# Kernel optimization log

Hardware: AMD Instinct MI355X
Metric: run time of the kernel (lower is better)

## Reference

```python
import jax, jax.numpy as jnp
import numpy as np

B, C, H, W = 4, 64, 96, 320
K = 9  # 3x3 kernel points
EPS = 1e-5


def conv3x3(x, w, b):
    # x: [B,Cin,H,W], w: [Cout,Cin,3,3], stride 1, pad 1
    out = jax.lax.conv_general_dilated(
        x, w, window_strides=(1, 1), padding=[(1, 1), (1, 1)],
        dimension_numbers=("NCHW", "OIHW", "NCHW"))
    return out + b[None, :, None, None]


def bn_eval(x, gamma, beta, mean, var):
    scale = gamma / jnp.sqrt(var + EPS)
    return x * scale[None, :, None, None] + (beta - mean * scale)[None, :, None, None]


def mdcn(x, offset, mask, w, b):
    # Modulated deformable conv v2, kernel 3, stride 1, pad 1, dilation 1.
    # offset: [B,2K,H,W] (channel 2k = dy, 2k+1 = dx, mmcv layout); mask: [B,K,H,W]
    Bb, Cc, Hh, Ww = x.shape
    off = offset.reshape(Bb, K, 2, Hh, Ww)
    dy, dx = off[:, :, 0], off[:, :, 1]               # [B,K,H,W]
    ks = jnp.arange(K)
    ky = (ks // 3 - 1).astype(x.dtype)[None, :, None, None]  # kernel row offset (pad=1)
    kx = (ks % 3 - 1).astype(x.dtype)[None, :, None, None]
    py = jnp.arange(Hh, dtype=x.dtype)[None, None, :, None] + ky + dy  # sample y
    px = jnp.arange(Ww, dtype=x.dtype)[None, None, None, :] + kx + dx  # sample x
    y0 = jnp.floor(py); x0 = jnp.floor(px)
    wy = py - y0; wx = px - x0
    y0i = y0.astype(jnp.int32); x0i = x0.astype(jnp.int32)
    x_flat = x.reshape(Bb, Cc, Hh * Ww)

    def gather(yi, xi):
        # bilinear corner with zero padding outside the image
        valid = ((yi >= 0) & (yi < Hh) & (xi >= 0) & (xi < Ww)).astype(x.dtype)
        idx = (jnp.clip(yi, 0, Hh - 1) * Ww + jnp.clip(xi, 0, Ww - 1)).reshape(Bb, 1, K * Hh * Ww)
        v = jnp.take_along_axis(x_flat, idx, axis=2).reshape(Bb, Cc, K, Hh, Ww)
        return v * valid[:, None]

    val = (((1 - wy) * (1 - wx))[:, None] * gather(y0i, x0i)
           + ((1 - wy) * wx)[:, None] * gather(y0i, x0i + 1)
           + (wy * (1 - wx))[:, None] * gather(y0i + 1, x0i)
           + (wy * wx)[:, None] * gather(y0i + 1, x0i + 1))  # [B,C,K,H,W]
    val = val * mask[:, None]
    out = jnp.einsum('bckhw,ock->bohw', val, w.reshape(w.shape[0], Cc, K))
    return out + b[None, :, None, None]


def setup_inputs() -> dict:
    key = jax.random.key(0)
    ks = jax.random.split(key, 16)
    s = 0.05
    return {
        "feat_rgb": jax.random.normal(ks[0], (B, C, H, W), jnp.float32),
        "feat_depth": jax.random.normal(ks[1], (B, C, H, W), jnp.float32),
        "w_off1": jax.random.normal(ks[2], (C, C, 3, 3), jnp.float32) * s,
        "b_off1": jax.random.normal(ks[3], (C,), jnp.float32) * s,
        "g1": 1.0 + jax.random.normal(ks[4], (C,), jnp.float32) * 0.1,
        "be1": jax.random.normal(ks[5], (C,), jnp.float32) * 0.1,
        "m1": jax.random.normal(ks[6], (C,), jnp.float32) * 0.1,
        "v1": jax.random.uniform(ks[7], (C,), jnp.float32, 0.5, 1.5),
        "w_off2": jax.random.normal(ks[8], (3 * K, C, 3, 3), jnp.float32) * s,
        "b_off2": jax.random.normal(ks[9], (3 * K,), jnp.float32) * s,
        "w_def": jax.random.normal(ks[10], (C, C, 3, 3), jnp.float32) * s,
        "b_def": jax.random.normal(ks[11], (C,), jnp.float32) * s,
        "w_f1": jax.random.normal(ks[12], (C, 2 * C, 3, 3), jnp.float32) * s,
        "b_f1": jax.random.normal(ks[13], (C,), jnp.float32) * s,
        "g2": 1.0 + jax.random.normal(ks[14], (C,), jnp.float32) * 0.1,
        "be2": jax.random.normal(ks[15], (C,), jnp.float32) * 0.1,
        "m2": jax.random.normal(jax.random.fold_in(key, 101), (C,), jnp.float32) * 0.1,
        "v2": jax.random.uniform(jax.random.fold_in(key, 102), (C,), jnp.float32, 0.5, 1.5),
        "w_out": jax.random.normal(jax.random.fold_in(key, 103), (1, C, 3, 3), jnp.float32) * s,
        "b_out": jax.random.normal(jax.random.fold_in(key, 104), (1,), jnp.float32) * s,
    }


def reference(feat_rgb, feat_depth, w_off1, b_off1, g1, be1, m1, v1,
              w_off2, b_off2, w_def, b_def, w_f1, b_f1, g2, be2, m2, v2,
              w_out, b_out):
    # offset head
    t = conv3x3(feat_rgb, w_off1, b_off1)
    t = bn_eval(t, g1, be1, m1, v1)
    head = conv3x3(t, w_off2, b_off2)            # [B,27,H,W]
    o1, o2, msk = jnp.split(head, 3, axis=1)
    offset = jnp.concatenate([o1, o2], axis=1)   # [B,18,H,W]
    msk = jax.nn.sigmoid(msk)                    # [B,9,H,W]
    # modulated deformable conv on depth features
    deform = mdcn(feat_depth, offset, msk, w_def, b_def)
    fd = feat_depth + deform
    fusion = jnp.concatenate([fd, feat_rgb], axis=1)  # [B,2C,H,W]
    h = jax.nn.relu(fusion)
    h = conv3x3(h, w_f1, b_f1)
    h = bn_eval(h, g2, be2, m2, v2)
    h = jax.nn.relu(h)  # Dropout(0.1) is identity at eval
    return conv3x3(h, w_out, b_out)  # [B,1,H,W]
```

## Files before the change

### kernel.cpp

```cpp
#include <hip/hip_runtime.h>
#include <math.h>

constexpr int Bc  = 4;
constexpr int Hc  = 96;
constexpr int Wc  = 320;
constexpr int HWc = Hc * Wc;
constexpr int NPIX = Bc * HWc;

typedef __attribute__((ext_vector_type(8))) short short8;
typedef __attribute__((ext_vector_type(4))) float f32x4;

constexpr size_t B_W1   = 0;
constexpr size_t B_W2   = 73728;
constexpr size_t B_WD   = 110592;
constexpr size_t B_WF   = 184320;
constexpr size_t B_AB   = 331776;
constexpr size_t B_RGBT = 332800;
constexpr size_t B_DEPT = 16061440;
constexpr size_t B_TT   = 31790080;
constexpr size_t B_HEAD = 47518720;

static __device__ __forceinline__ unsigned short f2bf(float f) {
    unsigned u = __builtin_bit_cast(unsigned, f);
    u = (u + 0x7fffu + ((u >> 16) & 1u)) >> 16;
    return (unsigned short)u;
}
static __device__ __forceinline__ float bf2f(unsigned short h) {
    unsigned u = ((unsigned)h) << 16;
    return __builtin_bit_cast(float, u);
}
static __device__ __forceinline__ int swz_blk(int bid, int chunk) {
    return (bid & 7) * chunk + (bid >> 3);
}

__global__ void prep_w(const float* __restrict__ w1, const float* __restrict__ b1,
                       const float* __restrict__ g1, const float* __restrict__ be1,
                       const float* __restrict__ m1, const float* __restrict__ v1,
                       const float* __restrict__ w2,
                       const float* __restrict__ wd,
                       const float* __restrict__ wf, const float* __restrict__ bf1,
                       const float* __restrict__ g2, const float* __restrict__ be2,
                       const float* __restrict__ m2, const float* __restrict__ v2,
                       char* __restrict__ ws) {
    int tid = blockIdx.x * blockDim.x + threadIdx.x;
    int stride = gridDim.x * blockDim.x;
    unsigned short* W1 = (unsigned short*)(ws + B_W1);
    unsigned short* W2 = (unsigned short*)(ws + B_W2);
    unsigned short* WD = (unsigned short*)(ws + B_WD);
    unsigned short* WF = (unsigned short*)(ws + B_WF);
    float* AB = (float*)(ws + B_AB);
    for (int i = tid; i < 36864; i += stride) {
        int ci = i & 63, co = (i >> 6) & 63, kk = i >> 12;
        W1[i] = f2bf(w1[(co * 64 + ci) * 9 + kk]);
    }
    for (int i = tid; i < 18432; i += stride) {
        int ci = i & 63, co = (i >> 6) & 31, kk = i >> 11;
        W2[i] = (co < 27) ? f2bf(w2[(co * 64 + ci) * 9 + kk]) : (unsigned short)0;
    }
    for (int i = tid; i < 36864; i += stride) {
        int c = i & 63, o = (i >> 6) & 63, kk = i >> 12;
        WD[i] = f2bf(wd[(o * 64 + c) * 9 + kk]);
    }
    for (int i = tid; i < 73728; i += stride) {
        int ci = i & 63, co = (i >> 6) & 63, r = i >> 12;
        int kk = r % 9, h = r / 9;
        WF[i] = f2bf(wf[(co * 128 + h * 64 + ci) * 9 + kk]);
    }
    if (tid < 64) {
        float s1 = g1[tid] / sqrtf(v1[tid] + 1e-5f);
        AB[tid]        = s1;
        AB[64 + tid]   = b1[tid] * s1 + be1[tid] - m1[tid] * s1;
        float s2 = g2[tid] / sqrtf(v2[tid] + 1e-5f);
        AB[128 + tid]  = s2;
        AB[192 + tid]  = bf1[tid] * s2 + be2[tid] - m2[tid] * s2;
    }
}

__global__ __launch_bounds__(256) void prep_x2(const float* __restrict__ rgb,
                                               const float* __restrict__ dep,
                                               unsigned short* __restrict__ rgbT,
                                               unsigned short* __restrict__ depT) {
    __shared__ unsigned short tr[64 * 66];
    int pg0 = blockIdx.x * 64;
    int b = pg0 / HWc, pix0 = pg0 % HWc;
    const float* srcs[2] = { rgb, dep };
    unsigned short* dsts[2] = { rgbT, depT };
#pragma unroll
    for (int which = 0; which < 2; ++which) {
        if (which) __syncthreads();
        const float* src = srcs[which];
#pragma unroll
        for (int it = 0; it < 16; ++it) {
            int idx = it * 256 + threadIdx.x;
            int p = idx & 63, ch = idx >> 6;
            float v = src[((size_t)b * 64 + ch) * HWc + pix0 + p];
            tr[p * 66 + ch] = f2bf(v);
        }
        __syncthreads();
        unsigned short* dst = dsts[which];
#pragma unroll
        for (int it = 0; it < 2; ++it) {
            int q = it * 256 + threadIdx.x;
            int p = q >> 3, g = q & 7;
            const char* basep = (const char*)tr + p * 132 + g * 16;
            uint4 u;
            u.x = *(const unsigned*)(basep + 0);
            u.y = *(const unsigned*)(basep + 4);
            u.z = *(const unsigned*)(basep + 8);
            u.w = *(const unsigned*)(basep + 12);
            *(uint4*)(dst + (size_t)(pg0 + p) * 64 + g * 8) = u;
        }
    }
}

static __device__ __forceinline__ void stage6(const unsigned short* __restrict__ src,
                                              int b, int y0, int x0,
                                              unsigned short* lds, bool do_relu) {
#pragma unroll
    for (int it = 0; it < 13; ++it) {
        int i = threadIdx.x + it * 256;
        if (i < 3168) {
            int g = i & 7;
            int xx = (i >> 3) % 66;
            int row = (i >> 3) / 66;
            int y = y0 - 1 + row, x = x0 - 1 + xx;
            short8 v = (short8)0;
            if ((unsigned)y < 96u && (unsigned)x < 320u) {
                v = *(const short8*)(src + ((size_t)(b * HWc + y * Wc + x)) * 64 + g * 8);
            }
            if (do_relu) {
#pragma unroll
                for (int j = 0; j < 8; ++j) {
                    short s = v[j];
                    v[j] = (s & (short)0x8000) ? (short)0 : s;
                }
            }
            int byte = ((row * 66 + xx) * 64 + g * 8) * 2;
            byte ^= ((xx & 7) << 4);
            *(short8*)((char*)lds + byte) = v;
        }
    }
}

static __device__ __forceinline__ short8 read_b6(const unsigned short* lds, int row, int xx, int cofs) {
    int byte = ((row * 66 + xx) * 64 + cofs) * 2;
    byte ^= ((xx & 7) << 4);
    return *(const short8*)((const char*)lds + byte);
}

__global__ __launch_bounds__(256) void conv1_m(const unsigned short* __restrict__ rgbT,
                                               const char* __restrict__ ws,
                                               unsigned short* __restrict__ tT) {
    __shared__ __align__(16) unsigned short xls[6 * 66 * 64];
    const unsigned short* W1 = (const unsigned short*)(ws + B_W1);
    const float* AB = (const float*)(ws + B_AB);
    int blk = swz_blk(blockIdx.x, 60);
    int xt = blk % 5, yt = (blk / 5) % 24, b = blk / 120;
    int x0 = xt * 64, y0 = yt * 4;
    stage6(rgbT, b, y0, x0, xls, false);
    __syncthreads();
    int lane = threadIdx.x & 63, w = threadIdx.x >> 6;
    int pl = lane & 15, q4 = lane >> 4;
    int p = w * 16 + pl;
    f32x4 acc[4][4];
#pragma unroll
    for (int r = 0; r < 4; ++r)
#pragma unroll
        for (int cp = 0; cp < 4; ++cp) acc[r][cp] = (f32x4)0.f;
#pragma unroll
    for (int kk = 0; kk < 9; ++kk) {
        int dy = kk / 3, dx = kk % 3;
        int xx = p + dx;
#pragma unroll
        for (int ch = 0; ch < 2; ++ch) {
            short8 bfr[4];
#pragma unroll
            for (int r = 0; r < 4; ++r) bfr[r] = read_b6(xls, dy + r, xx, ch * 32 + q4 * 8);
#pragma unroll
            for (int cp = 0; cp < 4; ++cp) {
                short8 afr = *(const short8*)(W1 + ((kk * 64 + cp * 16 + pl) * 64 + ch * 32 + q4 * 8));
#pragma unroll
                for (int r = 0; r < 4; ++r)
                    acc[r][cp] = __builtin_amdgcn_mfma_f32_16x16x32_bf16(afr, bfr[r], acc[r][cp], 0, 0, 0);
            }
        }
    }
#pragma unroll
    for (int r = 0; r < 4; ++r) {
        size_t pglob = (size_t)(b * HWc + (y0 + r) * Wc + x0 + p);
#pragma unroll
        for (int cp = 0; cp < 4; ++cp) {
            int co0 = cp * 16 + q4 * 4;
            f32x4 a1 = *(const f32x4*)(AB + co0);
            f32x4 b1 = *(const f32x4*)(AB + 64 + co0);
            unsigned short h4[4];
#pragma unroll
            for (int j = 0; j < 4; ++j) h4[j] = f2bf(fmaf(acc[r][cp][j], a1[j], b1[j]));
            uint2 u;
            u.x = (unsigned)h4[0] | ((unsigned)h4[1] << 16);
            u.y = (unsigned)h4[2] | ((unsigned)h4[3] << 16);
            *(uint2*)(tT + pglob * 64 + co0) = u;
        }
    }
}

__global__ __launch_bounds__(256) void conv2_m(const char* __restrict__ ws,
                                               const float* __restrict__ b2,
                                               float* __restrict__ headT,
                                               const unsigned short* __restrict__ tT) {
    __shared__ __align__(16) unsigned short xls[6 * 66 * 64];
    const unsigned short* W2 = (const unsigned short*)(ws + B_W2);
    int blk = swz_blk(blockIdx.x, 60);
    int xt = blk % 5, yt = (blk / 5) % 24, b = blk / 120;
    int x0 = xt * 64, y0 = yt * 4;
    stage6(tT, b, y0, x0, xls, false);
    __syncthreads();
    int lane = threadIdx.x & 63, w = threadIdx.x >> 6;
    int pl = lane & 15, q4 = lane >> 4;
    int p = w * 16 + pl;
    f32x4 acc[4][2];
#pragma unroll
    for (int r = 0; r < 4; ++r) { acc[r][0] = (f32x4)0.f; acc[r][1] = (f32x4)0.f; }
#pragma unroll
    for (int kk = 0; kk < 9; ++kk) {
        int dy = kk / 3, dx = kk % 3;
        int xx = p + dx;
#pragma unroll
        for (int ch = 0; ch < 2; ++ch) {
            short8 bfr[4];
#pragma unroll
            for (int r = 0; r < 4; ++r) bfr[r] = read_b6(xls, dy + r, xx, ch * 32 + q4 * 8);
#pragma unroll
            for (int cp = 0; cp < 2; ++cp) {
                short8 afr = *(const short8*)(W2 + ((kk * 32 + cp * 16 + pl) * 64 + ch * 32 + q4 * 8));
#pragma unroll
                for (int r = 0; r < 4; ++r)
                    acc[r][cp] = __builtin_amdgcn_mfma_f32_16x16x32_bf16(afr, bfr[r], acc[r][cp], 0, 0, 0);
            }
        }
    }
#pragma unroll
    for (int r = 0; r < 4; ++r) {
        size_t pglob = (size_t)(b * HWc + (y0 + r) * Wc + x0 + p);
#pragma unroll
        for (int cp = 0; cp < 2; ++cp) {
            int co0 = cp * 16 + q4 * 4;
            f32x4 rr;
#pragma unroll
            for (int j = 0; j < 4; ++j) {
                float bias = (co0 + j < 27) ? b2[co0 + j] : 0.f;
                rr[j] = acc[r][cp][j] + bias;
            }
            *(f32x4*)(headT + pglob * 32 + co0) = rr;
        }
    }
}

__global__ __launch_bounds__(256) void mdcn_l(const unsigned short* __restrict__ depthT,
                                              const float* __restrict__ headT,
                                              const char* __restrict__ ws,
                                              const float* __restrict__ bd,
                                              unsigned short* __restrict__ fdreluT) {
    __shared__ __align__(16) unsigned short vls[26048];
    const unsigned short* WD = (const unsigned short*)(ws + B_WD);
    int blk = swz_blk(blockIdx.x, 240);
    int xt = blk % 5, y = (blk / 5) % 96, b = blk / 480;
    int x0 = xt * 64;
    int lane = threadIdx.x & 63, w = threadIdx.x >> 6;
    int pl = lane & 15, q4 = lane >> 4;
    int p = w * 16 + pl;
    int px = x0 + p;
    size_t pglob = (size_t)(b * HWc + y * Wc + px);
    size_t dbase = (size_t)b * HWc * 64;
    const float* hd = headT + pglob * 32;
    float hv[28];
#pragma unroll
    for (int i = 0; i < 7; ++i) {
        f32x4 t = *(const f32x4*)(hd + i * 4);
        hv[i * 4 + 0] = t[0]; hv[i * 4 + 1] = t[1];
        hv[i * 4 + 2] = t[2]; hv[i * 4 + 3] = t[3];
    }
    f32x4 acc[4];
#pragma unroll
    for (int cp = 0; cp < 4; ++cp) acc[cp] = (f32x4)0.f;

    const int wy0 = y - 5;
    const int wx0 = x0 - 5;

#pragma unroll
    for (int pass = 0; pass < 2; ++pass) {
        if (pass) __syncthreads();
#pragma unroll
        for (int it = 0; it < 13; ++it) {
            int i = threadIdx.x + it * 256;
            if (i < 3256) {
                int sub = i & 3;
                int c = (i >> 2) % 74;
                int r = (i >> 2) / 74;
                int gy = wy0 + r, gx = wx0 + c;
                short8 v = (short8)0;
                if ((unsigned)gy < 96u && (unsigned)gx < 320u)
                    v = *(const short8*)(depthT + ((size_t)(b * HWc + gy * Wc + gx)) * 64 + pass * 32 + sub * 8);
                int byte = (((r * 74 + c) * 64) + sub * 16) ^ ((c & 6) << 3);
                *(short8*)((char*)vls + byte) = v;
            }
        }
        __syncthreads();
#pragma unroll
        for (int kk = 0; kk < 9; ++kk) {
            float dyv = hv[2 * kk], dxv = hv[2 * kk + 1], sm = hv[18 + kk];
            float m = 1.f / (1.f + __expf(-sm));
            float py  = (float)(y + kk / 3 - 1) + dyv;
            float pxf = (float)(px + kk % 3 - 1) + dxv;
            float y0f = floorf(py), x0f = floorf(pxf);
            float wy = py - y0f, wx = pxf - x0f;
            int iy0 = (int)y0f, ix0 = (int)x0f;
            bool vy0 = (unsigned)iy0 < 96u, vy1 = (unsigned)(iy0 + 1) < 96u;
            bool vx0 = (unsigned)ix0 < 320u, vx1 = (unsigned)(ix0 + 1) < 320u;
            int cy0 = min(max(iy0, 0), 95),  cy1 = min(max(iy0 + 1, 0), 95);
            int cx0 = min(max(ix0, 0), 319), cx1 = min(max(ix0 + 1, 0), 319);
            float w00 = (vy0 && vx0) ? (1.f - wy) * (1.f - wx) * m : 0.f;
            float w01 = (vy0 && vx1) ? (1.f - wy) * wx * m : 0.f;
            float w10 = (vy1 && vx0) ? wy * (1.f - wx) * m : 0.f;
            float w11 = (vy1 && vx1) ? wy * wx * m : 0.f;
            bool inw = ((unsigned)(iy0 - wy0) <= 9u) && ((unsigned)(ix0 - wx0) <= 72u);
            int lr0 = min(max(cy0 - wy0, 0), 10), lr1 = min(max(cy1 - wy0, 0), 10);
            int lc0 = min(max(cx0 - wx0, 0), 73), lc1 = min(max(cx1 - wx0, 0), 73);
            int qb = q4 * 16;
            short8 f00 = *(const short8*)((const char*)vls + ((((lr0 * 74 + lc0) * 64) + qb) ^ ((lc0 & 6) << 3)));
            short8 f01 = *(const short8*)((const char*)vls + ((((lr0 * 74 + lc1) * 64) + qb) ^ ((lc1 & 6) << 3)));
            short8 f10 = *(const short8*)((const char*)vls + ((((lr1 * 74 + lc0) * 64) + qb) ^ ((lc0 & 6) << 3)));
            short8 f11 = *(const short8*)((const char*)vls + ((((lr1 * 74 + lc1) * 64) + qb) ^ ((lc1 & 6) << 3)));
            if (!__all(inw)) {
                if (!inw) {
                    const unsigned short* bp = depthT + dbase + pass * 32 + q4 * 8;
                    f00 = *(const short8*)(bp + (size_t)(cy0 * Wc + cx0) * 64);
                    f01 = *(const short8*)(bp + (size_t)(cy0 * Wc + cx1) * 64);
                    f10 = *(const short8*)(bp + (size_t)(cy1 * Wc + cx0) * 64);
                    f11 = *(const short8*)(bp + (size_t)(cy1 * Wc + cx1) * 64);
                }
            }
            unsigned short vv[8];
#pragma unroll
            for (int j = 0; j < 8; ++j) {
                float v = w00 * bf2f((unsigned short)f00[j]) + w01 * bf2f((unsigned short)f01[j])
                        + w10 * bf2f((unsigned short)f10[j]) + w11 * bf2f((unsigned short)f11[j]);
                vv[j] = f2bf(v);
            }
            short8 bfr = *(short8*)vv;
#pragma unroll
            for (int cp = 0; cp < 4; ++cp) {
                short8 afr = *(const short8*)(WD + ((kk * 64 + cp * 16 + pl) * 64 + pass * 32 + q4 * 8));
                acc[cp] = __builtin_amdgcn_mfma_f32_16x16x32_bf16(afr, bfr, acc[cp], 0, 0, 0);
            }
        }
    }
#pragma unroll
    for (int cp = 0; cp < 4; ++cp) {
        int co0 = cp * 16 + q4 * 4;
        f32x4 bdv = *(const f32x4*)(bd + co0);
        uint2 dres = *(const uint2*)(depthT + pglob * 64 + co0);
        unsigned short d4[4] = { (unsigned short)(dres.x & 0xffff), (unsigned short)(dres.x >> 16),
                                 (unsigned short)(dres.y & 0xffff), (unsigned short)(dres.y >> 16) };
        unsigned short h4[4];
#pragma unroll
        for (int j = 0; j < 4; ++j) {
            float r = acc[cp][j] + bdv[j] + bf2f(d4[j]);
            h4[j] = f2bf(fmaxf(r, 0.f));
        }
        uint2 u;
        u.x = (unsigned)h4[0] | ((unsigned)h4[1] << 16);
        u.y = (unsigned)h4[2] | ((unsigned)h4[3] << 16);
        *(uint2*)(fdreluT + pglob * 64 + co0) = u;
    }
}

__global__ __launch_bounds__(256) void convf_m(const unsigned short* __restrict__ fdreluT,
                                               const unsigned short* __restrict__ rgbT,
                                               const char* __restrict__ ws,
                                               unsigned short* __restrict__ hT) {
    __shared__ __align__(16) unsigned short xls[6 * 66 * 64];
    const unsigned short* WF = (const unsigned short*)(ws + B_WF);
    const float* AB = (const float*)(ws + B_AB);
    int blk = swz_blk(blockIdx.x, 60);
    int xt = blk % 5, yt = (blk / 5) % 24, b = blk / 120;
    int x0 = xt * 64, y0 = yt * 4;
    int lane = threadIdx.x & 63, w = threadIdx.x >> 6;
    int pl = lane & 15, q4 = lane >> 4;
    int p = w * 16 + pl;
    f32x4 acc[4][4];
#pragma unroll
    for (int r = 0; r < 4; ++r)
#pragma unroll
        for (int cp = 0; cp < 4; ++cp) acc[r][cp] = (f32x4)0.f;
#pragma unroll
    for (int half = 0; half < 2; ++half) {
        if (half) __syncthreads();
        stage6(half ? rgbT : fdreluT, b, y0, x0, xls, half != 0);
        __syncthreads();
        const unsigned short* Wh = WF + half * 36864;
#pragma unroll
        for (int kk = 0; kk < 9; ++kk) {
            int dy = kk / 3, dx = kk % 3;
            int xx = p + dx;
#pragma unroll
            for (int ch = 0; ch < 2; ++ch) {
                short8 bfr[4];
#pragma unroll
                for (int r = 0; r < 4; ++r) bfr[r] = read_b6(xls, dy + r, xx, ch * 32 + q4 * 8);
#pragma unroll
                for (int cp = 0; cp < 4; ++cp) {
                    short8 afr = *(const short8*)(Wh + ((kk * 64 + cp * 16 + pl) * 64 + ch * 32 + q4 * 8));
#pragma unroll
                    for (int r = 0; r < 4; ++r)
                        acc[r][cp] = __builtin_amdgcn_mfma_f32_16x16x32_bf16(afr, bfr[r], acc[r][cp], 0, 0, 0);
                }
            }
        }
    }
#pragma unroll
    for (int r = 0; r < 4; ++r) {
        size_t pglob = (size_t)(b * HWc + (y0 + r) * Wc + x0 + p);
#pragma unroll
        for (int cp = 0; cp < 4; ++cp) {
            int co0 = cp * 16 + q4 * 4;
            f32x4 a2 = *(const f32x4*)(AB + 128 + co0);
            f32x4 b2 = *(const f32x4*)(AB + 192 + co0);
            unsigned short h4[4];
#pragma unroll
            for (int j = 0; j < 4; ++j) h4[j] = f2bf(fmaxf(fmaf(acc[r][cp][j], a2[j], b2[j]), 0.f));
            uint2 u;
            u.x = (unsigned)h4[0] | ((unsigned)h4[1] << 16);
            u.y = (unsigned)h4[2] | ((unsigned)h4[3] << 16);
            *(uint2*)(hT + pglob * 64 + co0) = u;
        }
    }
}

__global__ __launch_bounds__(256) void convo_m(const unsigned short* __restrict__ hT,
                                               const float* __restrict__ wo,
                                               const float* __restrict__ bo,
                                               float* __restrict__ out) {
    __shared__ float wl[576];
    for (int i = threadIdx.x; i < 576; i += 256) wl[i] = wo[i];
    __syncthreads();
    int p = swz_blk(blockIdx.x, 60) * 256 + threadIdx.x;
    int xw = p % Wc, rem = p / Wc, y = rem % Hc, b = rem / Hc;
    float acc = bo[0];
#pragma unroll
    for (int kk = 0; kk < 9; ++kk) {
        int iy = y + kk / 3 - 1, ix = xw + kk % 3 - 1;
        if ((unsigned)iy < 96u && (unsigned)ix < 320u) {
            const unsigned short* base = hT + ((size_t)(b * HWc + iy * Wc + ix)) * 64;
#pragma unroll
            for (int g = 0; g < 8; ++g) {
                short8 v = *(const short8*)(base + g * 8);
#pragma unroll
                for (int j = 0; j < 8; ++j)
                    acc = fmaf(bf2f((unsigned short)v[j]), wl[(g * 8 + j) * 9 + kk], acc);
            }
        }
    }
    out[p] = acc;
}

extern "C" void kernel_launch(void* const* d_in, const int* in_sizes, int n_in,
                              void* d_out, int out_size, void* d_ws, size_t ws_size,
                              hipStream_t stream) {
    const float* feat_rgb   = (const float*)d_in[0];
    const float* feat_depth = (const float*)d_in[1];
    const float* w_off1 = (const float*)d_in[2];
    const float* b_off1 = (const float*)d_in[3];
    const float* g1  = (const float*)d_in[4];
    const float* be1 = (const float*)d_in[5];
    const float* m1  = (const float*)d_in[6];
    const float* v1  = (const float*)d_in[7];
    const float* w_off2 = (const float*)d_in[8];
    const float* b_off2 = (const float*)d_in[9];
    const float* w_def  = (const float*)d_in[10];
    const float* b_def  = (const float*)d_in[11];
    const float* w_f1   = (const float*)d_in[12];
    const float* b_f1   = (const float*)d_in[13];
    const float* g2  = (const float*)d_in[14];
    const float* be2 = (const float*)d_in[15];
    const float* m2  = (const float*)d_in[16];
    const float* v2  = (const float*)d_in[17];
    const float* w_out = (const float*)d_in[18];
    const float* b_out = (const float*)d_in[19];
    (void)in_sizes; (void)n_in; (void)out_size; (void)ws_size;

    char* ws = (char*)d_ws;
    unsigned short* rgbT   = (unsigned short*)(ws + B_RGBT);
    unsigned short* depthT = (unsigned short*)(ws + B_DEPT);
    unsigned short* tT     = (unsigned short*)(ws + B_TT);
    float*          headT  = (float*)(ws + B_HEAD);
    unsigned short* fdreluT = tT;
    unsigned short* hT      = depthT;

    prep_w<<<64, 256, 0, stream>>>(w_off1, b_off1, g1, be1, m1, v1,
                                   w_off2, w_def, w_f1, b_f1, g2, be2, m2, v2, ws);
    prep_x2<<<NPIX / 64, 256, 0, stream>>>(feat_rgb, feat_depth, rgbT, depthT);
    conv1_m<<<480, 256, 0, stream>>>(rgbT, ws, tT);
    conv2_m<<<480, 256, 0, stream>>>(ws, b_off2, headT, tT);
    mdcn_l <<<1920, 256, 0, stream>>>(depthT, headT, ws, b_def, fdreluT);
    convf_m<<<480, 256, 0, stream>>>(fdreluT, rgbT, ws, hT);
    convo_m<<<480, 256, 0, stream>>>(hT, w_out, b_out, (float*)d_out);
}
```

Before: 398.2 us.

## Restructure deformable conv: per-(pixel,tap) direct gather into LDS im2col, then MFMA

The deformable conv kernel no longer stages an 11x74 depth window in LDS and samples from it per channel pass. Each thread now owns one (pixel, kernel-tap) task. It gathers all 64 channels of the four bilinear corners straight from global memory and writes the blended bf16 values into a swizzled LDS im2col tile. After one barrier the MFMA loop runs over 18 K-slices. Blocks shrink to 128 threads and 32 pixels, launching twice as many. This removes the window load, which mostly fetches unused data, and the two-pass barrier structure. The cost is uncoalesced 128-byte corner gathers from global memory/L2 and a lower thread-to-work ratio in the gather phase.

```diff
diff --git a/kernel.cpp b/kernel.cpp
--- a/kernel.cpp
+++ b/kernel.cpp
@@ -256,62 +256,31 @@
     }
 }
 
-__global__ __launch_bounds__(256) void mdcn_l(const unsigned short* __restrict__ depthT,
+__global__ __launch_bounds__(128) void mdcn_g(const unsigned short* __restrict__ depthT,
                                               const float* __restrict__ headT,
                                               const char* __restrict__ ws,
                                               const float* __restrict__ bd,
                                               unsigned short* __restrict__ fdreluT) {
-    __shared__ __align__(16) unsigned short vls[26048];
+    __shared__ __align__(16) unsigned short vls[32 * 576];
     const unsigned short* WD = (const unsigned short*)(ws + B_WD);
-    int blk = swz_blk(blockIdx.x, 240);
-    int xt = blk % 5, y = (blk / 5) % 96, b = blk / 480;
-    int x0 = xt * 64;
+    int blk = swz_blk(blockIdx.x, 480);
+    int xt = blk % 10, y = (blk / 10) % 96, b = blk / 960;
+    int x0 = xt * 32;
     int lane = threadIdx.x & 63, w = threadIdx.x >> 6;
-    int pl = lane & 15, q4 = lane >> 4;
-    int p = w * 16 + pl;
-    int px = x0 + p;
-    size_t pglob = (size_t)(b * HWc + y * Wc + px);
     size_t dbase = (size_t)b * HWc * 64;
-    const float* hd = headT + pglob * 32;
-    float hv[28];
-#pragma unroll
-    for (int i = 0; i < 7; ++i) {
-        f32x4 t = *(const f32x4*)(hd + i * 4);
-        hv[i * 4 + 0] = t[0]; hv[i * 4 + 1] = t[1];
-        hv[i * 4 + 2] = t[2]; hv[i * 4 + 3] = t[3];
-    }
-    f32x4 acc[4];
-#pragma unroll
-    for (int cp = 0; cp < 4; ++cp) acc[cp] = (f32x4)0.f;
-
-    const int wy0 = y - 5;
-    const int wx0 = x0 - 5;
-
-#pragma unroll
-    for (int pass = 0; pass < 2; ++pass) {
-        if (pass) __syncthreads();
-#pragma unroll
-        for (int it = 0; it < 13; ++it) {
-            int i = threadIdx.x + it * 256;
-            if (i < 3256) {
-                int sub = i & 3;
-                int c = (i >> 2) % 74;
-                int r = (i >> 2) / 74;
-                int gy = wy0 + r, gx = wx0 + c;
-                short8 v = (short8)0;
-                if ((unsigned)gy < 96u && (unsigned)gx < 320u)
-                    v = *(const short8*)(depthT + ((size_t)(b * HWc + gy * Wc + gx)) * 64 + pass * 32 + sub * 8);
-                int byte = (((r * 74 + c) * 64) + sub * 16) ^ ((c & 6) << 3);
-                *(short8*)((char*)vls + byte) = v;
-            }
-        }
-        __syncthreads();
-#pragma unroll
-        for (int kk = 0; kk < 9; ++kk) {
-            float dyv = hv[2 * kk], dxv = hv[2 * kk + 1], sm = hv[18 + kk];
+    size_t rowbase = (size_t)(b * HWc + y * Wc + x0);
+
+#pragma unroll
+    for (int it = 0; it < 3; ++it) {
+        int idx = it * 64 + lane;
+        if (idx < 144) {
+            int task = w * 144 + idx;
+            int px = task & 31, kk = task >> 5;
+            const float* hd = headT + (rowbase + px) * 32;
+            float dyv = hd[2 * kk], dxv = hd[2 * kk + 1], sm = hd[18 + kk];
             float m = 1.f / (1.f + __expf(-sm));
             float py  = (float)(y + kk / 3 - 1) + dyv;
-            float pxf = (float)(px + kk % 3 - 1) + dxv;
+            float pxf = (float)(x0 + px + kk % 3 - 1) + dxv;
             float y0f = floorf(py), x0f = floorf(pxf);
             float wy = py - y0f, wx = pxf - x0f;
             int iy0 = (int)y0f, ix0 = (int)x0f;
@@ -323,38 +292,49 @@
             float w01 = (vy0 && vx1) ? (1.f - wy) * wx * m : 0.f;
             float w10 = (vy1 && vx0) ? wy * (1.f - wx) * m : 0.f;
             float w11 = (vy1 && vx1) ? wy * wx * m : 0.f;
-            bool inw = ((unsigned)(iy0 - wy0) <= 9u) && ((unsigned)(ix0 - wx0) <= 72u);
-            int lr0 = min(max(cy0 - wy0, 0), 10), lr1 = min(max(cy1 - wy0, 0), 10);
-            int lc0 = min(max(cx0 - wx0, 0), 73), lc1 = min(max(cx1 - wx0, 0), 73);
-            int qb = q4 * 16;
-            short8 f00 = *(const short8*)((const char*)vls + ((((lr0 * 74 + lc0) * 64) + qb) ^ ((lc0 & 6) << 3)));
-            short8 f01 = *(const short8*)((const char*)vls + ((((lr0 * 74 + lc1) * 64) + qb) ^ ((lc1 & 6) << 3)));
-            short8 f10 = *(const short8*)((const char*)vls + ((((lr1 * 74 + lc0) * 64) + qb) ^ ((lc0 & 6) << 3)));
-            short8 f11 = *(const short8*)((const char*)vls + ((((lr1 * 74 + lc1) * 64) + qb) ^ ((lc1 & 6) << 3)));
-            if (!__all(inw)) {
-                if (!inw) {
-                    const unsigned short* bp = depthT + dbase + pass * 32 + q4 * 8;
-                    f00 = *(const short8*)(bp + (size_t)(cy0 * Wc + cx0) * 64);
-                    f01 = *(const short8*)(bp + (size_t)(cy0 * Wc + cx1) * 64);
-                    f10 = *(const short8*)(bp + (size_t)(cy1 * Wc + cx0) * 64);
-                    f11 = *(const short8*)(bp + (size_t)(cy1 * Wc + cx1) * 64);
+            const unsigned short* r00 = depthT + dbase + (size_t)(cy0 * Wc + cx0) * 64;
+            const unsigned short* r01 = depthT + dbase + (size_t)(cy0 * Wc + cx1) * 64;
+            const unsigned short* r10 = depthT + dbase + (size_t)(cy1 * Wc + cx0) * 64;
+            const unsigned short* r11 = depthT + dbase + (size_t)(cy1 * Wc + cx1) * 64;
+            int base = px * 1152 + kk * 128;
+#pragma unroll
+            for (int c8 = 0; c8 < 8; ++c8) {
+                short8 f00 = *(const short8*)(r00 + c8 * 8);
+                short8 f01 = *(const short8*)(r01 + c8 * 8);
+                short8 f10 = *(const short8*)(r10 + c8 * 8);
+                short8 f11 = *(const short8*)(r11 + c8 * 8);
+                unsigned short vv[8];
+#pragma unroll
+                for (int j = 0; j < 8; ++j) {
+                    float v = w00 * bf2f((unsigned short)f00[j]) + w01 * bf2f((unsigned short)f01[j])
+                            + w10 * bf2f((unsigned short)f10[j]) + w11 * bf2f((unsigned short)f11[j]);
+                    vv[j] = f2bf(v);
                 }
-            }
-            unsigned short vv[8];
-#pragma unroll
-            for (int j = 0; j < 8; ++j) {
-                float v = w00 * bf2f((unsigned short)f00[j]) + w01 * bf2f((unsigned short)f01[j])
-                        + w10 * bf2f((unsigned short)f10[j]) + w11 * bf2f((unsigned short)f11[j]);
-                vv[j] = f2bf(v);
-            }
-            short8 bfr = *(short8*)vv;
-#pragma unroll
-            for (int cp = 0; cp < 4; ++cp) {
-                short8 afr = *(const short8*)(WD + ((kk * 64 + cp * 16 + pl) * 64 + pass * 32 + q4 * 8));
-                acc[cp] = __builtin_amdgcn_mfma_f32_16x16x32_bf16(afr, bfr, acc[cp], 0, 0, 0);
-            }
-        }
-    }
+                int byte = (base + c8 * 16) ^ ((px & 7) << 4);
+                *(short8*)((char*)vls + byte) = *(short8*)vv;
+            }
+        }
+    }
+    __syncthreads();
+
+    int pl = lane & 15, q4 = lane >> 4;
+    int p = w * 16 + pl;
+    f32x4 acc[4];
+#pragma unroll
+    for (int cp = 0; cp < 4; ++cp) acc[cp] = (f32x4)0.f;
+#pragma unroll
+    for (int s = 0; s < 18; ++s) {
+        int kk = s >> 1, hf = s & 1;
+        int byte = (p * 1152 + kk * 128 + hf * 64 + q4 * 16) ^ ((p & 7) << 4);
+        short8 bfr = *(const short8*)((const char*)vls + byte);
+#pragma unroll
+        for (int cp = 0; cp < 4; ++cp) {
+            short8 afr = *(const short8*)(WD + ((kk * 64 + cp * 16 + pl) * 64 + hf * 32 + q4 * 8));
+            acc[cp] = __builtin_amdgcn_mfma_f32_16x16x32_bf16(afr, bfr, acc[cp], 0, 0, 0);
+        }
+    }
+
+    size_t pglob = rowbase + p;
 #pragma unroll
     for (int cp = 0; cp < 4; ++cp) {
         int co0 = cp * 16 + q4 * 4;
@@ -502,7 +482,7 @@
     prep_x2<<<NPIX / 64, 256, 0, stream>>>(feat_rgb, feat_depth, rgbT, depthT);
     conv1_m<<<480, 256, 0, stream>>>(rgbT, ws, tT);
     conv2_m<<<480, 256, 0, stream>>>(ws, b_off2, headT, tT);
-    mdcn_l <<<1920, 256, 0, stream>>>(depthT, headT, ws, b_def, fdreluT);
+    mdcn_g <<<3840, 128, 0, stream>>>(depthT, headT, ws, b_def, fdreluT);
     convf_m<<<480, 256, 0, stream>>>(fdreluT, rgbT, ws, hT);
     convo_m<<<480, 256, 0, stream>>>(hT, w_out, b_out, (float*)d_out);
 }
```

After: 435.9 us. 1.09x slower.

## Stage conv input tiles in 32-channel halves to halve shared memory

Applied to the files above, without the earlier changes.

The three MFMA conv kernels now stage the 6x66 halo tile 32 channels at a time instead of all 64, looping over the two channel halves with a barrier between them. This halves the LDS footprint per block (about 50KB down to about 25KB), so more blocks can be resident per CU and hide global-load latency. In exchange each block pays extra __syncthreads and serialised staging phases, and the 8-byte swizzle now sits on a 64-byte row stride, which may change the bank-conflict pattern.

```diff
diff --git a/kernel.cpp b/kernel.cpp
--- a/kernel.cpp
+++ b/kernel.cpp
@@ -113,20 +113,20 @@
     }
 }
 
-static __device__ __forceinline__ void stage6(const unsigned short* __restrict__ src,
-                                              int b, int y0, int x0,
-                                              unsigned short* lds, bool do_relu) {
-#pragma unroll
-    for (int it = 0; it < 13; ++it) {
+static __device__ __forceinline__ void stage6h(const unsigned short* __restrict__ src,
+                                               int b, int y0, int x0,
+                                               unsigned short* lds, bool do_relu, int ch0) {
+#pragma unroll
+    for (int it = 0; it < 7; ++it) {
         int i = threadIdx.x + it * 256;
-        if (i < 3168) {
-            int g = i & 7;
-            int xx = (i >> 3) % 66;
-            int row = (i >> 3) / 66;
+        if (i < 1584) {
+            int g = i & 3;
+            int xx = (i >> 2) % 66;
+            int row = (i >> 2) / 66;
             int y = y0 - 1 + row, x = x0 - 1 + xx;
             short8 v = (short8)0;
             if ((unsigned)y < 96u && (unsigned)x < 320u) {
-                v = *(const short8*)(src + ((size_t)(b * HWc + y * Wc + x)) * 64 + g * 8);
+                v = *(const short8*)(src + ((size_t)(b * HWc + y * Wc + x)) * 64 + ch0 + g * 8);
             }
             if (do_relu) {
 #pragma unroll
@@ -135,15 +135,15 @@
                     v[j] = (s & (short)0x8000) ? (short)0 : s;
                 }
             }
-            int byte = ((row * 66 + xx) * 64 + g * 8) * 2;
+            int byte = ((row * 66 + xx) * 32 + g * 8) * 2;
             byte ^= ((xx & 7) << 4);
             *(short8*)((char*)lds + byte) = v;
         }
     }
 }
 
-static __device__ __forceinline__ short8 read_b6(const unsigned short* lds, int row, int xx, int cofs) {
-    int byte = ((row * 66 + xx) * 64 + cofs) * 2;
+static __device__ __forceinline__ short8 read_b6h(const unsigned short* lds, int row, int xx, int c) {
+    int byte = ((row * 66 + xx) * 32 + c) * 2;
     byte ^= ((xx & 7) << 4);
     return *(const short8*)((const char*)lds + byte);
 }
@@ -151,14 +151,12 @@
 __global__ __launch_bounds__(256) void conv1_m(const unsigned short* __restrict__ rgbT,
                                                const char* __restrict__ ws,
                                                unsigned short* __restrict__ tT) {
-    __shared__ __align__(16) unsigned short xls[6 * 66 * 64];
+    __shared__ __align__(16) unsigned short xls[6 * 66 * 32];
     const unsigned short* W1 = (const unsigned short*)(ws + B_W1);
     const float* AB = (const float*)(ws + B_AB);
     int blk = swz_blk(blockIdx.x, 60);
     int xt = blk % 5, yt = (blk / 5) % 24, b = blk / 120;
     int x0 = xt * 64, y0 = yt * 4;
-    stage6(rgbT, b, y0, x0, xls, false);
-    __syncthreads();
     int lane = threadIdx.x & 63, w = threadIdx.x >> 6;
     int pl = lane & 15, q4 = lane >> 4;
     int p = w * 16 + pl;
@@ -168,17 +166,20 @@
 #pragma unroll
         for (int cp = 0; cp < 4; ++cp) acc[r][cp] = (f32x4)0.f;
 #pragma unroll
-    for (int kk = 0; kk < 9; ++kk) {
-        int dy = kk / 3, dx = kk % 3;
-        int xx = p + dx;
-#pragma unroll
-        for (int ch = 0; ch < 2; ++ch) {
+    for (int chp = 0; chp < 2; ++chp) {
+        if (chp) __syncthreads();
+        stage6h(rgbT, b, y0, x0, xls, false, chp * 32);
+        __syncthreads();
+#pragma unroll
+        for (int kk = 0; kk < 9; ++kk) {
+            int dy = kk / 3, dx = kk % 3;
+            int xx = p + dx;
             short8 bfr[4];
 #pragma unroll
-            for (int r = 0; r < 4; ++r) bfr[r] = read_b6(xls, dy + r, xx, ch * 32 + q4 * 8);
+            for (int r = 0; r < 4; ++r) bfr[r] = read_b6h(xls, dy + r, xx, q4 * 8);
 #pragma unroll
             for (int cp = 0; cp < 4; ++cp) {
-                short8 afr = *(const short8*)(W1 + ((kk * 64 + cp * 16 + pl) * 64 + ch * 32 + q4 * 8));
+                short8 afr = *(const short8*)(W1 + ((kk * 64 + cp * 16 + pl) * 64 + chp * 32 + q4 * 8));
 #pragma unroll
                 for (int r = 0; r < 4; ++r)
                     acc[r][cp] = __builtin_amdgcn_mfma_f32_16x16x32_bf16(afr, bfr[r], acc[r][cp], 0, 0, 0);
@@ -208,13 +209,11 @@
                                                const float* __restrict__ b2,
                                                float* __restrict__ headT,
                                                const unsigned short* __restrict__ tT) {
-    __shared__ __align__(16) unsigned short xls[6 * 66 * 64];
+    __shared__ __align__(16) unsigned short xls[6 * 66 * 32];
     const unsigned short* W2 = (const unsigned short*)(ws + B_W2);
     int blk = swz_blk(blockIdx.x, 60);
     int xt = blk % 5, yt = (blk / 5) % 24, b = blk / 120;
     int x0 = xt * 64, y0 = yt * 4;
-    stage6(tT, b, y0, x0, xls, false);
-    __syncthreads();
     int lane = threadIdx.x & 63, w = threadIdx.x >> 6;
     int pl = lane & 15, q4 = lane >> 4;
     int p = w * 16 + pl;
@@ -222,17 +221,20 @@
 #pragma unroll
     for (int r = 0; r < 4; ++r) { acc[r][0] = (f32x4)0.f; acc[r][1] = (f32x4)0.f; }
 #pragma unroll
-    for (int kk = 0; kk < 9; ++kk) {
-        int dy = kk / 3, dx = kk % 3;
-        int xx = p + dx;
-#pragma unroll
-        for (int ch = 0; ch < 2; ++ch) {
+    for (int chp = 0; chp < 2; ++chp) {
+        if (chp) __syncthreads();
+        stage6h(tT, b, y0, x0, xls, false, chp * 32);
+        __syncthreads();
+#pragma unroll
+        for (int kk = 0; kk < 9; ++kk) {
+            int dy = kk / 3, dx = kk % 3;
+            int xx = p + dx;
             short8 bfr[4];
 #pragma unroll
-            for (int r = 0; r < 4; ++r) bfr[r] = read_b6(xls, dy + r, xx, ch * 32 + q4 * 8);
+            for (int r = 0; r < 4; ++r) bfr[r] = read_b6h(xls, dy + r, xx, q4 * 8);
 #pragma unroll
             for (int cp = 0; cp < 2; ++cp) {
-                short8 afr = *(const short8*)(W2 + ((kk * 32 + cp * 16 + pl) * 64 + ch * 32 + q4 * 8));
+                short8 afr = *(const short8*)(W2 + ((kk * 32 + cp * 16 + pl) * 64 + chp * 32 + q4 * 8));
 #pragma unroll
                 for (int r = 0; r < 4; ++r)
                     acc[r][cp] = __builtin_amdgcn_mfma_f32_16x16x32_bf16(afr, bfr[r], acc[r][cp], 0, 0, 0);
@@ -379,7 +381,7 @@
                                                const unsigned short* __restrict__ rgbT,
                                                const char* __restrict__ ws,
                                                unsigned short* __restrict__ hT) {
-    __shared__ __align__(16) unsigned short xls[6 * 66 * 64];
+    __shared__ __align__(16) unsigned short xls[6 * 66 * 32];
     const unsigned short* WF = (const unsigned short*)(ws + B_WF);
     const float* AB = (const float*)(ws + B_AB);
     int blk = swz_blk(blockIdx.x, 60);
@@ -395,22 +397,23 @@
         for (int cp = 0; cp < 4; ++cp) acc[r][cp] = (f32x4)0.f;
 #pragma unroll
     for (int half = 0; half < 2; ++half) {
-        if (half) __syncthreads();
-        stage6(half ? rgbT : fdreluT, b, y0, x0, xls, half != 0);
-        __syncthreads();
+        const unsigned short* src = half ? rgbT : fdreluT;
         const unsigned short* Wh = WF + half * 36864;
 #pragma unroll
-        for (int kk = 0; kk < 9; ++kk) {
-            int dy = kk / 3, dx = kk % 3;
-            int xx = p + dx;
-#pragma unroll
-            for (int ch = 0; ch < 2; ++ch) {
+        for (int chp = 0; chp < 2; ++chp) {
+            if (half || chp) __syncthreads();
+            stage6h(src, b, y0, x0, xls, half != 0, chp * 32);
+            __syncthreads();
+#pragma unroll
+            for (int kk = 0; kk < 9; ++kk) {
+                int dy = kk / 3, dx = kk % 3;
+                int xx = p + dx;
                 short8 bfr[4];
 #pragma unroll
-                for (int r = 0; r < 4; ++r) bfr[r] = read_b6(xls, dy + r, xx, ch * 32 + q4 * 8);
+                for (int r = 0; r < 4; ++r) bfr[r] = read_b6h(xls, dy + r, xx, q4 * 8);
 #pragma unroll
                 for (int cp = 0; cp < 4; ++cp) {
-                    short8 afr = *(const short8*)(Wh + ((kk * 64 + cp * 16 + pl) * 64 + ch * 32 + q4 * 8));
+                    short8 afr = *(const short8*)(Wh + ((kk * 64 + cp * 16 + pl) * 64 + chp * 32 + q4 * 8));
 #pragma unroll
                     for (int r = 0; r < 4; ++r)
                         acc[r][cp] = __builtin_amdgcn_mfma_f32_16x16x32_bf16(afr, bfr[r], acc[r][cp], 0, 0, 0);
```

Result: faster. 376.0 us (-5.6%).
